# Kernel optimization log

Measured on AMD Instinct MI355X. Metric: run time of the kernel, lower is better.

Reference implementation:

```python
import jax, jax.numpy as jnp
import numpy as np

LN_EPS = 1e-5
L2_EPS = 1e-12
SCALE = 1.0 / np.sqrt(768.0)
TOPK = 8


def _ln(x, g, b):
    m = jnp.mean(x, axis=-1, keepdims=True)
    v = jnp.mean(jnp.square(x - m), axis=-1, keepdims=True)
    return (x - m) * jax.lax.rsqrt(v + LN_EPS) * g + b


def _l2norm(x):
    n = jnp.sqrt(jnp.sum(jnp.square(x), axis=-1, keepdims=True))
    return x / jnp.maximum(n, L2_EPS)


def _topk_normalize(scores, k):
    # scores: [B, K]; keep top-k, zero rest, renormalize to sum 1
    vals, idx = jax.lax.top_k(scores, k)
    B = scores.shape[0]
    weights = jnp.zeros_like(scores).at[jnp.arange(B)[:, None], idx].set(vals)
    denom = jnp.maximum(jnp.sum(weights, axis=1, keepdims=True), 1e-8)
    return weights / denom


def setup_inputs() -> dict:
    key = jax.random.key(0)
    ks = jax.random.split(key, 8)
    B, N, D, K, H, C = 32, 4096, 768, 64, 3072, 1000
    inp = {
        "patch_tokens": jax.random.normal(ks[0], (B, N, D), jnp.float32),
        "global_features": jax.random.normal(ks[1], (B, D), jnp.float32),
        "base_logits": jax.random.normal(ks[2], (B, C), jnp.float32),
        "bq": jax.random.normal(ks[3], (K, D), jnp.float32) * 0.02,
        "qn_g": jnp.ones((D,)), "qn_b": jnp.zeros((D,)),
        "tn_g": jnp.ones((D,)), "tn_b": jnp.zeros((D,)),
        "bn_g": jnp.ones((D,)), "bn_b": jnp.zeros((D,)),
        "gn_g": jnp.ones((D,)), "gn_b": jnp.zeros((D,)),
        "rln_g": jnp.ones((D,)), "rln_b": jnp.zeros((D,)),
        "rw1": jax.random.normal(ks[4], (D, H), jnp.float32) / np.sqrt(D),
        "rb1": jnp.zeros((H,)),
        "rw2": jax.random.normal(ks[5], (H, 1), jnp.float32) / np.sqrt(H),
        "rb2": jnp.zeros((1,)),
        "hw1": jax.random.normal(ks[6], (2 * D, H), jnp.float32) / np.sqrt(2 * D),
        "hb1": jnp.zeros((H,)),
        "hw2": jax.random.normal(ks[7], (H, C), jnp.float32) / np.sqrt(H),
        "hb2": jnp.zeros((C,)),
    }
    return inp


def reference(patch_tokens, global_features, base_logits, bq,
              qn_g, qn_b, tn_g, tn_b, bn_g, bn_b, gn_g, gn_b,
              rln_g, rln_b, rw1, rb1, rw2, rb2, hw1, hb1, hw2, hb2):
    # normalized cross-attention: K basis queries vs N tokens
    tokens_key = _l2norm(_ln(patch_tokens, tn_g, tn_b))           # [B,N,D]
    queries = _l2norm(_ln(bq, qn_g, qn_b))                        # [K,D]
    attn_logits = jnp.einsum('kd,bnd->bkn', queries, tokens_key) * SCALE
    attn_weights = jax.nn.softmax(attn_logits, axis=-1)           # [B,K,N]
    basis_states = jnp.einsum('bkn,bnd->bkd', attn_weights, patch_tokens)
    # routing head: LN -> Linear -> GELU -> Linear -> softplus
    r = _ln(basis_states, rln_g, rln_b)
    r = jax.nn.gelu(r @ rw1 + rb1, approximate=False)
    routing_scores = jax.nn.softplus((r @ rw2 + rb2)[..., 0])     # [B,K]
    routing_weights = _topk_normalize(routing_scores, TOPK)
    basis_summary = jnp.einsum('bk,bkd->bd', routing_weights, basis_states)
    basis_summary = _ln(basis_summary, bn_g, bn_b)
    global_summary = _ln(global_features, gn_g, gn_b)
    fused = jnp.concatenate([global_summary, basis_summary], axis=-1)
    h = jax.nn.gelu(fused @ hw1 + hb1, approximate=False)
    residual_logits = h @ hw2 + hb2
    final_logits = base_logits + residual_logits
    # diversity loss over basis queries
    bqn = _l2norm(bq)
    gram = bqn @ bqn.T
    diversity_loss = jnp.mean(jnp.square(gram - jnp.eye(gram.shape[0], dtype=gram.dtype)))
    sparse_loss = jnp.mean(routing_scores)
    return (final_logits, residual_logits, routing_weights, sparse_loss, diversity_loss)
```

## Files before the change

### kernel.cpp

```cpp
#include <hip/hip_runtime.h>
#include <math.h>

#define SCALE 0.036084391824351613f

typedef unsigned short us;
typedef __attribute__((ext_vector_type(8))) short short8;
typedef __attribute__((ext_vector_type(4))) short short4s;
typedef __attribute__((ext_vector_type(4))) float f32x4;
#define MFMA16(a, b, c) __builtin_amdgcn_mfma_f32_16x16x32_bf16(a, b, c, 0, 0, 0)

__device__ __forceinline__ us f2bf(float f) {
  unsigned u = __float_as_uint(f);
  unsigned r = (u + 0x7fffu + ((u >> 16) & 1u)) >> 16;
  return (us)r;
}
__device__ __forceinline__ float bf2f(us u) { return __uint_as_float(((unsigned)u) << 16); }

__device__ __forceinline__ void split8(f32x4 a, f32x4 b, short8& hi, short8& lo) {
  float x[8] = {a[0], a[1], a[2], a[3], b[0], b[1], b[2], b[3]};
#pragma unroll
  for (int i = 0; i < 8; i++) {
    us h = f2bf(x[i]);
    hi[i] = (short)h;
    lo[i] = (short)f2bf(x[i] - bf2f(h));
  }
}

__device__ __forceinline__ float blockReduceSum(float v, float* sh) {
#pragma unroll
  for (int o = 32; o > 0; o >>= 1) v += __shfl_xor(v, o, 64);
  int lane = threadIdx.x & 63, wid = threadIdx.x >> 6;
  __syncthreads();
  if (lane == 0) sh[wid] = v;
  __syncthreads();
  float r = sh[0];
  int nw = blockDim.x >> 6;
  for (int i = 1; i < nw; i++) r += sh[i];
  return r;
}

__device__ __forceinline__ float blockReduceMax(float v, float* sh) {
#pragma unroll
  for (int o = 32; o > 0; o >>= 1) v = fmaxf(v, __shfl_xor(v, o, 64));
  int lane = threadIdx.x & 63, wid = threadIdx.x >> 6;
  __syncthreads();
  if (lane == 0) sh[wid] = v;
  __syncthreads();
  float r = sh[0];
  int nw = blockDim.x >> 6;
  for (int i = 1; i < nw; i++) r = fmaxf(r, sh[i]);
  return r;
}

__device__ __forceinline__ float gelu_exact(float x) {
  return 0.5f * x * (1.0f + erff(x * 0.7071067811865476f));
}

__global__ void __launch_bounds__(256) k_prep_queries(
    const float* __restrict__ bq, const float* __restrict__ qn_g, const float* __restrict__ qn_b,
    const float* __restrict__ tn_g, const float* __restrict__ tn_b,
    us* __restrict__ qgh, us* __restrict__ qgl,
    float* __restrict__ s1, float* __restrict__ qb,
    float* __restrict__ bqn, float* __restrict__ gcons) {
  __shared__ float sh[8];
  int k = blockIdx.x, t = threadIdx.x;
  const float* xr = bq + (size_t)k * 768;
  float x0 = xr[t], x1 = xr[t + 256], x2 = xr[t + 512];
  float sx = blockReduceSum(x0 + x1 + x2, sh);
  float sxx = blockReduceSum(x0 * x0 + x1 * x1 + x2 * x2, sh);
  float mean = sx * (1.0f / 768.0f);
  float var = fmaxf(sxx * (1.0f / 768.0f) - mean * mean, 0.0f);
  float rs = rsqrtf(var + 1e-5f);
  float y0 = (x0 - mean) * rs * qn_g[t] + qn_b[t];
  float y1 = (x1 - mean) * rs * qn_g[t + 256] + qn_b[t + 256];
  float y2 = (x2 - mean) * rs * qn_g[t + 512] + qn_b[t + 512];
  float ss = blockReduceSum(y0 * y0 + y1 * y1 + y2 * y2, sh);
  float inv = 1.0f / fmaxf(sqrtf(ss), 1e-12f);
  float q0 = y0 * inv, q1 = y1 * inv, q2 = y2 * inv;
  float tg0 = tn_g[t], tg1 = tn_g[t + 256], tg2 = tn_g[t + 512];
  float tb0 = tn_b[t], tb1 = tn_b[t + 256], tb2 = tn_b[t + 512];
  float g0 = q0 * tg0, g1 = q1 * tg1, g2 = q2 * tg2;
  us h0 = f2bf(g0), h1 = f2bf(g1), h2 = f2bf(g2);
  qgh[(size_t)k * 768 + t] = h0;
  qgh[(size_t)k * 768 + t + 256] = h1;
  qgh[(size_t)k * 768 + t + 512] = h2;
  qgl[(size_t)k * 768 + t] = f2bf(g0 - bf2f(h0));
  qgl[(size_t)k * 768 + t + 256] = f2bf(g1 - bf2f(h1));
  qgl[(size_t)k * 768 + t + 512] = f2bf(g2 - bf2f(h2));
  float s1p = blockReduceSum(g0 + g1 + g2, sh);
  float qbp = blockReduceSum(q0 * tb0 + q1 * tb1 + q2 * tb2, sh);
  if (t == 0) { s1[k] = s1p; qb[k] = qbp; }
  float inv2 = 1.0f / fmaxf(sqrtf(sxx), 1e-12f);
  bqn[(size_t)k * 768 + t] = x0 * inv2;
  bqn[(size_t)k * 768 + t + 256] = x1 * inv2;
  bqn[(size_t)k * 768 + t + 512] = x2 * inv2;
  float sggp = blockReduceSum(tg0 * tg0 + tg1 * tg1 + tg2 * tg2, sh);
  float sgbp = blockReduceSum(tg0 * tb0 + tg1 * tb1 + tg2 * tb2, sh);
  float sbbp = blockReduceSum(tb0 * tb0 + tb1 * tb1 + tb2 * tb2, sh);
  if (k == 0 && t == 0) { gcons[0] = sggp; gcons[1] = sgbp; gcons[2] = sbbp; }
}

__global__ void __launch_bounds__(256) k_gram(const float* __restrict__ bqn,
                                              float* __restrict__ gpart) {
  __shared__ float bk[768];
  __shared__ float arr[64];
  int k = blockIdx.x, t = threadIdx.x;
  bk[t] = bqn[(size_t)k * 768 + t];
  bk[t + 256] = bqn[(size_t)k * 768 + t + 256];
  bk[t + 512] = bqn[(size_t)k * 768 + t + 512];
  __syncthreads();
  int j = t >> 2, sub = t & 3;
  const float* bj = bqn + (size_t)j * 768 + sub * 192;
  float v = 0.0f;
  for (int d = 0; d < 192; d++) v += bk[sub * 192 + d] * bj[d];
  v += __shfl_xor(v, 1, 64);
  v += __shfl_xor(v, 2, 64);
  if (sub == 0) { float e = v - (j == k ? 1.0f : 0.0f); arr[j] = e * e; }
  __syncthreads();
  if (t < 64) {
    float s = arr[t];
#pragma unroll
    for (int o = 32; o > 0; o >>= 1) s += __shfl_xor(s, o, 64);
    if (t == 0) gpart[k] = s;
  }
}

__global__ void __launch_bounds__(256) k_w1t(const float* __restrict__ rw1,
                                             us* __restrict__ w1th, us* __restrict__ w1tl) {
  __shared__ float tl[32][33];
  int d0 = blockIdx.x * 32, h0 = blockIdx.y * 32;
  int t = threadIdx.x, tx = t & 31, ty = t >> 5;
#pragma unroll
  for (int j = 0; j < 4; j++)
    tl[ty + j * 8][tx] = rw1[(size_t)(d0 + ty + j * 8) * 3072 + h0 + tx];
  __syncthreads();
#pragma unroll
  for (int j = 0; j < 4; j++) {
    float v = tl[tx][ty + j * 8];
    us h = f2bf(v);
    w1th[(size_t)(h0 + ty + j * 8) * 768 + d0 + tx] = h;
    w1tl[(size_t)(h0 + ty + j * 8) * 768 + d0 + tx] = f2bf(v - bf2f(h));
  }
}

__global__ void __launch_bounds__(256) k_attn_mfma(
    const float* __restrict__ x, const us* __restrict__ qgh, const us* __restrict__ qgl,
    const float* __restrict__ s1v, const float* __restrict__ qbv,
    const float* __restrict__ tng, const float* __restrict__ tnb,
    const float* __restrict__ gcons, float* __restrict__ L) {
  __shared__ __align__(16) us qsh[64 * 32], qsl[64 * 32];
  __shared__ __align__(16) us xsh[128 * 32], xsl[128 * 32];
  __shared__ float sA[128], sB[128], sC[128];
  const int b = blockIdx.y, n0 = blockIdx.x * 128;
  const int t = threadIdx.x, w = t >> 6, l = t & 63;
  const int sr = t >> 2, sq = t & 3;
  const us* qsrcH = qgh + (size_t)sr * 768 + sq * 8;
  const us* qsrcL = qgl + (size_t)sr * 768 + sq * 8;
  const float* xsrc = x + ((size_t)b * 4096 + n0 + sr) * 768 + sq * 8;
  f32x4 acc[4][2];
#pragma unroll
  for (int i = 0; i < 4; i++)
#pragma unroll
    for (int j = 0; j < 2; j++) acc[i][j] = (f32x4){0.f, 0.f, 0.f, 0.f};
  float s0x = 0, s0xx = 0, s0a = 0, s0b = 0, s0c = 0;
  float t1x = 0, t1xx = 0, t1a = 0, t1b = 0, t1c = 0;
  short8 qh = *(const short8*)qsrcH, ql = *(const short8*)qsrcL;
  f32x4 x0a = *(const f32x4*)xsrc, x0b = *(const f32x4*)(xsrc + 4);
  f32x4 x1a = *(const f32x4*)(xsrc + (size_t)64 * 768);
  f32x4 x1b = *(const f32x4*)(xsrc + (size_t)64 * 768 + 4);
  for (int dk = 0; dk < 768; dk += 32) {
    f32x4 ga = *(const f32x4*)(tng + dk + sq * 8);
    f32x4 gA = *(const f32x4*)(tng + dk + sq * 8 + 4);
    f32x4 ba = *(const f32x4*)(tnb + dk + sq * 8);
    f32x4 bA = *(const f32x4*)(tnb + dk + sq * 8 + 4);
#pragma unroll
    for (int i = 0; i < 4; i++) {
      float g1 = ga[i], g2 = gA[i], b1 = ba[i], b2 = bA[i];
      float xv = x0a[i]; float gx = g1 * xv;
      s0x += xv; s0xx = fmaf(xv, xv, s0xx);
      s0a = fmaf(gx, gx, s0a); s0b = fmaf(g1, gx, s0b); s0c = fmaf(b1, gx, s0c);
      xv = x0b[i]; gx = g2 * xv;
      s0x += xv; s0xx = fmaf(xv, xv, s0xx);
      s0a = fmaf(gx, gx, s0a); s0b = fmaf(g2, gx, s0b); s0c = fmaf(b2, gx, s0c);
      xv = x1a[i]; gx = g1 * xv;
      t1x += xv; t1xx = fmaf(xv, xv, t1xx);
      t1a = fmaf(gx, gx, t1a); t1b = fmaf(g1, gx, t1b); t1c = fmaf(b1, gx, t1c);
      xv = x1b[i]; gx = g2 * xv;
      t1x += xv; t1xx = fmaf(xv, xv, t1xx);
      t1a = fmaf(gx, gx, t1a); t1b = fmaf(g2, gx, t1b); t1c = fmaf(b2, gx, t1c);
    }
    short8 hi, lo;
    __syncthreads();
    *(short8*)&qsh[sr * 32 + sq * 8] = qh; *(short8*)&qsl[sr * 32 + sq * 8] = ql;
    split8(x0a, x0b, hi, lo);
    *(short8*)&xsh[sr * 32 + sq * 8] = hi; *(short8*)&xsl[sr * 32 + sq * 8] = lo;
    split8(x1a, x1b, hi, lo);
    *(short8*)&xsh[(sr + 64) * 32 + sq * 8] = hi; *(short8*)&xsl[(sr + 64) * 32 + sq * 8] = lo;
    __syncthreads();
    if (dk + 32 < 768) {
      int d2 = dk + 32;
      qh = *(const short8*)(qsrcH + d2); ql = *(const short8*)(qsrcL + d2);
      x0a = *(const f32x4*)(xsrc + d2); x0b = *(const f32x4*)(xsrc + d2 + 4);
      x1a = *(const f32x4*)(xsrc + (size_t)64 * 768 + d2);
      x1b = *(const f32x4*)(xsrc + (size_t)64 * 768 + d2 + 4);
    }
    short8 ah[4], al[4];
#pragma unroll
    for (int kt = 0; kt < 4; kt++) {
      int off = (kt * 16 + (l & 15)) * 32 + (l >> 4) * 8;
      ah[kt] = *(const short8*)&qsh[off];
      al[kt] = *(const short8*)&qsl[off];
    }
#pragma unroll
    for (int nt = 0; nt < 2; nt++) {
      int off = (w * 32 + nt * 16 + (l & 15)) * 32 + (l >> 4) * 8;
      short8 bh = *(const short8*)&xsh[off];
      short8 bl = *(const short8*)&xsl[off];
#pragma unroll
      for (int kt = 0; kt < 4; kt++) {
        acc[kt][nt] = MFMA16(ah[kt], bh, acc[kt][nt]);
        acc[kt][nt] = MFMA16(ah[kt], bl, acc[kt][nt]);
        acc[kt][nt] = MFMA16(al[kt], bh, acc[kt][nt]);
        acc[kt][nt] = MFMA16(al[kt], bl, acc[kt][nt]);
      }
    }
  }
  float sgg = gcons[0], sgb = gcons[1], sbb = gcons[2];
#define R4(v) v += __shfl_xor(v, 1, 64); v += __shfl_xor(v, 2, 64)
  R4(s0x); R4(s0xx); R4(s0a); R4(s0b); R4(s0c);
  R4(t1x); R4(t1xx); R4(t1a); R4(t1b); R4(t1c);
#undef R4
  if (sq == 0) {
    {
      float m = s0x * (1.0f / 768.0f);
      float var = fmaxf(s0xx * (1.0f / 768.0f) - m * m, 0.0f);
      float rs = rsqrtf(var + 1e-5f);
      float ss = fmaxf(rs * rs * (s0a - 2.0f * m * s0b + m * m * sgg) +
                       2.0f * rs * (s0c - m * sgb) + sbb, 0.0f);
      float inv = 1.0f / fmaxf(sqrtf(ss), 1e-12f);
      float A = SCALE * inv * rs;
      sA[sr] = A; sB[sr] = A * m; sC[sr] = SCALE * inv;
    }
    {
      float m = t1x * (1.0f / 768.0f);
      float var = fmaxf(t1xx * (1.0f / 768.0f) - m * m, 0.0f);
      float rs = rsqrtf(var + 1e-5f);
      float ss = fmaxf(rs * rs * (t1a - 2.0f * m * t1b + m * m * sgg) +
                       2.0f * rs * (t1c - m * sgb) + sbb, 0.0f);
      float inv = 1.0f / fmaxf(sqrtf(ss), 1e-12f);
      float A = SCALE * inv * rs;
      sA[sr + 64] = A; sB[sr + 64] = A * m; sC[sr + 64] = SCALE * inv;
    }
  }
  __syncthreads();
#pragma unroll
  for (int nt = 0; nt < 2; nt++) {
    int nn = w * 32 + nt * 16 + (l & 15);
    int n = n0 + nn;
    float Av = sA[nn], Bv = sB[nn], Cv = sC[nn];
#pragma unroll
    for (int kt = 0; kt < 4; kt++) {
#pragma unroll
      for (int r = 0; r < 4; r++) {
        int k = kt * 16 + (l >> 4) * 4 + r;
        L[((size_t)b * 64 + k) * 4096 + n] = Av * acc[kt][nt][r] - Bv * s1v[k] + Cv * qbv[k];
      }
    }
  }
}

__global__ void __launch_bounds__(256) k_rowstat(const float* __restrict__ L,
                                                 float* __restrict__ rowm,
                                                 float* __restrict__ rowinv) {
  __shared__ float sh[8];
  size_t row = blockIdx.x;
  const f32x4* p = (const f32x4*)(L + row * 4096);
  int t = threadIdx.x;
  f32x4 v[4];
  float mx = -INFINITY;
#pragma unroll
  for (int i = 0; i < 4; i++) {
    v[i] = p[t + i * 256];
#pragma unroll
    for (int j = 0; j < 4; j++) mx = fmaxf(mx, v[i][j]);
  }
  mx = blockReduceMax(mx, sh);
  float s = 0.0f;
#pragma unroll
  for (int i = 0; i < 4; i++)
#pragma unroll
    for (int j = 0; j < 4; j++) s += expf(v[i][j] - mx);
  s = blockReduceSum(s, sh);
  if (t == 0) { rowm[row] = mx; rowinv[row] = 1.0f / s; }
}

__global__ void __launch_bounds__(256) k_zero(float* __restrict__ p) {
  ((f32x4*)p)[blockIdx.x * 256 + threadIdx.x] = (f32x4){0.f, 0.f, 0.f, 0.f};
}

__global__ void __launch_bounds__(256) k_pv_mfma(
    const float* __restrict__ x, const float* __restrict__ W,
    const float* __restrict__ rowm, const float* __restrict__ rowinv,
    float* __restrict__ S) {
  __shared__ __align__(16) us wth[64 * 32], wtl[64 * 32];
  __shared__ __align__(16) us xth[8 * 32 * 16], xtl[8 * 32 * 16];
  const int b = blockIdx.y, d0 = blockIdx.x * 128, nb = blockIdx.z * 512;
  const int t = threadIdx.x, w = t >> 6, l = t & 63;
  const int krow = t >> 2;
  const float* wsrc = W + ((size_t)b * 64 + krow) * 4096 + nb + (t & 3) * 8;
  const float mr = rowm[b * 64 + krow];
  const float ir = rowinv[b * 64 + krow];
  const int gg = t >> 6, nn = (t >> 1) & 31, hh = t & 1;
  const float* xsrc0 = x + ((size_t)b * 4096 + nb + nn) * 768 + d0 + gg * 16 + hh * 8;
  const float* xsrc1 = xsrc0 + 64;
  f32x4 acc[4][2];
#pragma unroll
  for (int i = 0; i < 4; i++)
#pragma unroll
    for (int j = 0; j < 2; j++) acc[i][j] = (f32x4){0.f, 0.f, 0.f, 0.f};
  f32x4 w0a = *(const f32x4*)wsrc, w0b = *(const f32x4*)(wsrc + 4);
  f32x4 xa0 = *(const f32x4*)xsrc0, xb0 = *(const f32x4*)(xsrc0 + 4);
  f32x4 xa1 = *(const f32x4*)xsrc1, xb1 = *(const f32x4*)(xsrc1 + 4);
  for (int ns = 0; ns < 512; ns += 32) {
    short8 hi, lo;
    f32x4 e0, e1;
#pragma unroll
    for (int i = 0; i < 4; i++) {
      e0[i] = expf(w0a[i] - mr) * ir;
      e1[i] = expf(w0b[i] - mr) * ir;
    }
    __syncthreads();
    split8(e0, e1, hi, lo);
    *(short8*)&wth[krow * 32 + (t & 3) * 8] = hi;
    *(short8*)&wtl[krow * 32 + (t & 3) * 8] = lo;
    split8(xa0, xb0, hi, lo);
    *(short8*)&xth[(size_t)t * 8] = hi; *(short8*)&xtl[(size_t)t * 8] = lo;
    split8(xa1, xb1, hi, lo);
    *(short8*)&xth[((size_t)t + 256) * 8] = hi; *(short8*)&xtl[((size_t)t + 256) * 8] = lo;
    __syncthreads();
    if (ns + 32 < 512) {
      w0a = *(const f32x4*)(wsrc + ns + 32); w0b = *(const f32x4*)(wsrc + ns + 36);
      const float* p0 = xsrc0 + (size_t)(ns + 32) * 768;
      xa0 = *(const f32x4*)p0; xb0 = *(const f32x4*)(p0 + 4);
      xa1 = *(const f32x4*)(p0 + 64); xb1 = *(const f32x4*)(p0 + 68);
    }
    short8 ah[4], al[4];
#pragma unroll
    for (int kt = 0; kt < 4; kt++) {
      int off = (kt * 16 + (l & 15)) * 32 + (l >> 4) * 8;
      ah[kt] = *(const short8*)&wth[off];
      al[kt] = *(const short8*)&wtl[off];
    }
#pragma unroll
    for (int dt = 0; dt < 2; dt++) {
      const us* gph = &xth[(2 * w + dt) * 512];
      const us* gpl = &xtl[(2 * w + dt) * 512];
      int rb = (l >> 4) * 8, cc = l & 15;
      short8 bh, bl;
#pragma unroll
      for (int i = 0; i < 8; i++) {
        bh[i] = (short)gph[(rb + i) * 16 + cc];
        bl[i] = (short)gpl[(rb + i) * 16 + cc];
      }
#pragma unroll
      for (int kt = 0; kt < 4; kt++) {
        acc[kt][dt] = MFMA16(ah[kt], bh, acc[kt][dt]);
        acc[kt][dt] = MFMA16(ah[kt], bl, acc[kt][dt]);
        acc[kt][dt] = MFMA16(al[kt], bh, acc[kt][dt]);
        acc[kt][dt] = MFMA16(al[kt], bl, acc[kt][dt]);
      }
    }
  }
#pragma unroll
  for (int dt = 0; dt < 2; dt++) {
    int d = d0 + w * 32 + dt * 16 + (l & 15);
#pragma unroll
    for (int kt = 0; kt < 4; kt++) {
#pragma unroll
      for (int r = 0; r < 4; r++) {
        int k = kt * 16 + (l >> 4) * 4 + r;
        atomicAdd(&S[((size_t)b * 64 + k) * 768 + d], acc[kt][dt][r]);
      }
    }
  }
}

__global__ void __launch_bounds__(256) k_ln768(
    const float* __restrict__ in, const float* __restrict__ g, const float* __restrict__ b,
    us* __restrict__ outh, us* __restrict__ outl) {
  int wid = threadIdx.x >> 6, lane = threadIdx.x & 63;
  size_t row = (size_t)blockIdx.x * 4 + wid;
  const f32x4* xr = (const f32x4*)(in + row * 768);
  f32x4 v[3];
  float sx = 0, sxx = 0;
#pragma unroll
  for (int j = 0; j < 3; j++) {
    v[j] = xr[lane + j * 64];
#pragma unroll
    for (int i = 0; i < 4; i++) { sx += v[j][i]; sxx = fmaf(v[j][i], v[j][i], sxx); }
  }
#pragma unroll
  for (int o = 32; o > 0; o >>= 1) { sx += __shfl_xor(sx, o, 64); sxx += __shfl_xor(sxx, o, 64); }
  float mean = sx * (1.0f / 768.0f);
  float var = fmaxf(sxx * (1.0f / 768.0f) - mean * mean, 0.0f);
  float rs = rsqrtf(var + 1e-5f);
  const f32x4* gp = (const f32x4*)g;
  const f32x4* bp = (const f32x4*)b;
#pragma unroll
  for (int j = 0; j < 3; j++) {
    f32x4 gv = gp[lane + j * 64], bv = bp[lane + j * 64];
    short4s h4, l4;
#pragma unroll
    for (int i = 0; i < 4; i++) {
      float y = (v[j][i] - mean) * rs * gv[i] + bv[i];
      us h = f2bf(y);
      h4[i] = (short)h;
      l4[i] = (short)f2bf(y - bf2f(h));
    }
    int e = (lane + j * 64) * 4;
    *(short4s*)&outh[row * 768 + e] = h4;
    *(short4s*)&outl[row * 768 + e] = l4;
  }
}

__global__ void __launch_bounds__(256) k_rh_mfma(
    const us* __restrict__ rhh, const us* __restrict__ rhl,
    const us* __restrict__ w1th, const us* __restrict__ w1tl,
    const float* __restrict__ rb1, const float* __restrict__ rw2,
    float* __restrict__ scores_raw) {
  __shared__ __align__(16) us ash[64 * 32], asl[64 * 32];
  __shared__ __align__(16) us bsh[128 * 32], bsl[128 * 32];
  __shared__ float spart[4][64];
  const int h0 = blockIdx.x * 128, m0 = blockIdx.y * 64;
  const int t = threadIdx.x, w = t >> 6, l = t & 63;
  const int sr = t >> 2, sq = t & 3;
  const us* aH = rhh + (size_t)(m0 + sr) * 768 + sq * 8;
  const us* aL = rhl + (size_t)(m0 + sr) * 768 + sq * 8;
  const us* bH = w1th + (size_t)(h0 + sr) * 768 + sq * 8;
  const us* bL = w1tl + (size_t)(h0 + sr) * 768 + sq * 8;
  f32x4 acc[4][2];
#pragma unroll
  for (int i = 0; i < 4; i++)
#pragma unroll
    for (int j = 0; j < 2; j++) acc[i][j] = (f32x4){0.f, 0.f, 0.f, 0.f};
  short8 a0h = *(const short8*)aH, a0l = *(const short8*)aL;
  short8 b0h = *(const short8*)bH, b0l = *(const short8*)bL;
  short8 b1h = *(const short8*)(bH + (size_t)64 * 768);
  short8 b1l = *(const short8*)(bL + (size_t)64 * 768);
  for (int dk = 0; dk < 768; dk += 32) {
    __syncthreads();
    *(short8*)&ash[sr * 32 + sq * 8] = a0h; *(short8*)&asl[sr * 32 + sq * 8] = a0l;
    *(short8*)&bsh[sr * 32 + sq * 8] = b0h; *(short8*)&bsl[sr * 32 + sq * 8] = b0l;
    *(short8*)&bsh[(sr + 64) * 32 + sq * 8] = b1h; *(short8*)&bsl[(sr + 64) * 32 + sq * 8] = b1l;
    __syncthreads();
    if (dk + 32 < 768) {
      int d2 = dk + 32;
      a0h = *(const short8*)(aH + d2); a0l = *(const short8*)(aL + d2);
      b0h = *(const short8*)(bH + d2); b0l = *(const short8*)(bL + d2);
      b1h = *(const short8*)(bH + (size_t)64 * 768 + d2);
      b1l = *(const short8*)(bL + (size_t)64 * 768 + d2);
    }
    short8 ah[4], al[4];
#pragma unroll
    for (int kt = 0; kt < 4; kt++) {
      int off = (kt * 16 + (l & 15)) * 32 + (l >> 4) * 8;
      ah[kt] = *(const short8*)&ash[off];
      al[kt] = *(const short8*)&asl[off];
    }
#pragma unroll
    for (int nt = 0; nt < 2; nt++) {
      int off = (w * 32 + nt * 16 + (l & 15)) * 32 + (l >> 4) * 8;
      short8 bh = *(const short8*)&bsh[off];
      short8 bl = *(const short8*)&bsl[off];
#pragma unroll
      for (int kt = 0; kt < 4; kt++) {
        acc[kt][nt] = MFMA16(ah[kt], bh, acc[kt][nt]);
        acc[kt][nt] = MFMA16(ah[kt], bl, acc[kt][nt]);
        acc[kt][nt] = MFMA16(al[kt], bh, acc[kt][nt]);
        acc[kt][nt] = MFMA16(al[kt], bl, acc[kt][nt]);
      }
    }
  }
  float psum[4][4];
#pragma unroll
  for (int kt = 0; kt < 4; kt++)
#pragma unroll
    for (int r = 0; r < 4; r++) psum[kt][r] = 0.f;
#pragma unroll
  for (int nt = 0; nt < 2; nt++) {
    int h = h0 + w * 32 + nt * 16 + (l & 15);
    float bias = rb1[h];
    float rw2v = rw2[h];
#pragma unroll
    for (int kt = 0; kt < 4; kt++) {
#pragma unroll
      for (int r = 0; r < 4; r++) {
        float g = gelu_exact(acc[kt][nt][r] + bias);
        psum[kt][r] = fmaf(g, rw2v, psum[kt][r]);
      }
    }
  }
#pragma unroll
  for (int kt = 0; kt < 4; kt++)
#pragma unroll
    for (int r = 0; r < 4; r++) {
      float v = psum[kt][r];
      v += __shfl_xor(v, 1, 64);
      v += __shfl_xor(v, 2, 64);
      v += __shfl_xor(v, 4, 64);
      v += __shfl_xor(v, 8, 64);
      psum[kt][r] = v;
    }
  if ((l & 15) == 0) {
#pragma unroll
    for (int kt = 0; kt < 4; kt++)
#pragma unroll
      for (int r = 0; r < 4; r++)
        spart[w][kt * 16 + (l >> 4) * 4 + r] = psum[kt][r];
  }
  __syncthreads();
  if (t < 64)
    atomicAdd(&scores_raw[m0 + t], spart[0][t] + spart[1][t] + spart[2][t] + spart[3][t]);
}

__global__ void __launch_bounds__(256) k_fused(
    const float* __restrict__ bs, const float* __restrict__ scores_raw,
    const float* __restrict__ rb2, const float* __restrict__ gf,
    const float* __restrict__ bn_g, const float* __restrict__ bn_b,
    const float* __restrict__ gn_g, const float* __restrict__ gn_b,
    float* __restrict__ fused, float* __restrict__ rw_out) {
  __shared__ float sh[8];
  __shared__ float wsh[64];
  int b = blockIdx.x, t = threadIdx.x;
  if (t < 64) {
    float z = scores_raw[b * 64 + t] + rb2[0];
    float s = fmaxf(z, 0.0f) + log1pf(expf(-fabsf(z)));
    bool sel = false;
    for (int it = 0; it < 8; it++) {
      float v = sel ? -INFINITY : s;
      int idx = t;
#pragma unroll
      for (int o = 32; o > 0; o >>= 1) {
        float v2 = __shfl_xor(v, o, 64);
        int i2 = __shfl_xor(idx, o, 64);
        if (v2 > v || (v2 == v && i2 < idx)) { v = v2; idx = i2; }
      }
      if (t == idx) sel = true;
    }
    float wv = sel ? s : 0.0f;
    float tot = wv;
#pragma unroll
    for (int o = 32; o > 0; o >>= 1) tot += __shfl_xor(tot, o, 64);
    float wt = wv / fmaxf(tot, 1e-8f);
    wsh[t] = wt;
    rw_out[b * 64 + t] = wt;
  }
  __syncthreads();
  float v0 = 0, v1 = 0, v2 = 0;
  const float* bsb = bs + (size_t)b * 64 * 768;
  for (int k = 0; k < 64; k++) {
    float w = wsh[k];
    if (w != 0.0f) {
      v0 = fmaf(w, bsb[(size_t)k * 768 + t], v0);
      v1 = fmaf(w, bsb[(size_t)k * 768 + t + 256], v1);
      v2 = fmaf(w, bsb[(size_t)k * 768 + t + 512], v2);
    }
  }
  float sx = blockReduceSum(v0 + v1 + v2, sh);
  float sxx = blockReduceSum(v0 * v0 + v1 * v1 + v2 * v2, sh);
  float mean = sx * (1.0f / 768.0f);
  float var = fmaxf(sxx * (1.0f / 768.0f) - mean * mean, 0.0f);
  float rs = rsqrtf(var + 1e-5f);
  float* fb = fused + (size_t)b * 1536;
  fb[768 + t] = (v0 - mean) * rs * bn_g[t] + bn_b[t];
  fb[768 + t + 256] = (v1 - mean) * rs * bn_g[t + 256] + bn_b[t + 256];
  fb[768 + t + 512] = (v2 - mean) * rs * bn_g[t + 512] + bn_b[t + 512];
  const float* gr = gf + (size_t)b * 768;
  float g0 = gr[t], g1 = gr[t + 256], g2 = gr[t + 512];
  float gsx = blockReduceSum(g0 + g1 + g2, sh);
  float gsxx = blockReduceSum(g0 * g0 + g1 * g1 + g2 * g2, sh);
  float gm = gsx * (1.0f / 768.0f);
  float gv = fmaxf(gsxx * (1.0f / 768.0f) - gm * gm, 0.0f);
  float grs = rsqrtf(gv + 1e-5f);
  fb[t] = (g0 - gm) * grs * gn_g[t] + gn_b[t];
  fb[t + 256] = (g1 - gm) * grs * gn_g[t + 256] + gn_b[t + 256];
  fb[t + 512] = (g2 - gm) * grs * gn_g[t + 512] + gn_b[t + 512];
}

__global__ void __launch_bounds__(256) k_head1(
    const float* __restrict__ fused, const float* __restrict__ hw1, const float* __restrict__ hb1,
    float* __restrict__ h) {
  __shared__ float fl[2][1536];
  __shared__ float part[2][4][64];
  int bp = blockIdx.y * 2, h0 = blockIdx.x * 64, t = threadIdx.x;
  for (int i = t; i < 1536; i += 256) {
    fl[0][i] = fused[(size_t)bp * 1536 + i];
    fl[1][i] = fused[(size_t)(bp + 1) * 1536 + i];
  }
  __syncthreads();
  int c = t & 63, sl = t >> 6;
  int hh = h0 + c;
  int kbase = sl * 384;
  const float* wp = hw1 + (size_t)kbase * 3072 + hh;
  float a0 = 0.f, a1 = 0.f;
#pragma unroll 8
  for (int k = 0; k < 384; k++) {
    float w = wp[(size_t)k * 3072];
    a0 = fmaf(fl[0][kbase + k], w, a0);
    a1 = fmaf(fl[1][kbase + k], w, a1);
  }
  part[0][sl][c] = a0; part[1][sl][c] = a1;
  __syncthreads();
  if (sl == 0) {
    float bias = hb1[hh];
    float s0 = part[0][0][c] + part[0][1][c] + part[0][2][c] + part[0][3][c];
    float s1_ = part[1][0][c] + part[1][1][c] + part[1][2][c] + part[1][3][c];
    h[(size_t)bp * 3072 + hh] = gelu_exact(s0 + bias);
    h[(size_t)(bp + 1) * 3072 + hh] = gelu_exact(s1_ + bias);
  }
}

__global__ void __launch_bounds__(256) k_head2(
    const float* __restrict__ h, const float* __restrict__ hw2, const float* __restrict__ hb2,
    const float* __restrict__ base, float* __restrict__ out) {
  __shared__ float hl[2][3072];
  __shared__ float part[2][4][64];
  int bp = blockIdx.y * 2, c0 = blockIdx.x * 64, t = threadIdx.x;
  for (int i = t; i < 3072; i += 256) {
    hl[0][i] = h[(size_t)bp * 3072 + i];
    hl[1][i] = h[(size_t)(bp + 1) * 3072 + i];
  }
  __syncthreads();
  int c = t & 63, sl = t >> 6;
  int cc = c0 + c;
  int csafe = cc < 1000 ? cc : 999;
  int kbase = sl * 768;
  const float* wp = hw2 + (size_t)kbase * 1000 + csafe;
  float a0 = 0.f, a1 = 0.f;
#pragma unroll 8
  for (int k = 0; k < 768; k++) {
    float w = wp[(size_t)k * 1000];
    a0 = fmaf(hl[0][kbase + k], w, a0);
    a1 = fmaf(hl[1][kbase + k], w, a1);
  }
  part[0][sl][c] = a0; part[1][sl][c] = a1;
  __syncthreads();
  if (sl == 0 && cc < 1000) {
    float bias = hb2[cc];
    float s0 = part[0][0][c] + part[0][1][c] + part[0][2][c] + part[0][3][c] + bias;
    float s1_ = part[1][0][c] + part[1][1][c] + part[1][2][c] + part[1][3][c] + bias;
    out[32000 + bp * 1000 + cc] = s0;
    out[bp * 1000 + cc] = base[bp * 1000 + cc] + s0;
    out[32000 + (bp + 1) * 1000 + cc] = s1_;
    out[(bp + 1) * 1000 + cc] = base[(bp + 1) * 1000 + cc] + s1_;
  }
}

__global__ void __launch_bounds__(256) k_losses(
    const float* __restrict__ scores_raw, const float* __restrict__ rb2,
    const float* __restrict__ gpart, float* __restrict__ out) {
  __shared__ float sh[8];
  int t = threadIdx.x;
  float s = 0.0f;
#pragma unroll
  for (int i = 0; i < 8; i++) {
    float z = scores_raw[t + i * 256] + rb2[0];
    s += fmaxf(z, 0.0f) + log1pf(expf(-fabsf(z)));
  }
  s = blockReduceSum(s, sh);
  float gsum = (t < 64) ? gpart[t] : 0.0f;
  gsum = blockReduceSum(gsum, sh);
  if (t == 0) {
    out[66048] = s * (1.0f / 2048.0f);
    out[66049] = gsum * (1.0f / 4096.0f);
  }
}

extern "C" void kernel_launch(void* const* d_in, const int* in_sizes, int n_in,
                              void* d_out, int out_size, void* d_ws, size_t ws_size,
                              hipStream_t stream) {
  const float* patch = (const float*)d_in[0];
  const float* gfeat = (const float*)d_in[1];
  const float* base  = (const float*)d_in[2];
  const float* bq    = (const float*)d_in[3];
  const float* qn_g  = (const float*)d_in[4];
  const float* qn_b  = (const float*)d_in[5];
  const float* tn_g  = (const float*)d_in[6];
  const float* tn_b  = (const float*)d_in[7];
  const float* bn_g  = (const float*)d_in[8];
  const float* bn_b  = (const float*)d_in[9];
  const float* gn_g  = (const float*)d_in[10];
  const float* gn_b  = (const float*)d_in[11];
  const float* rln_g = (const float*)d_in[12];
  const float* rln_b = (const float*)d_in[13];
  const float* rw1   = (const float*)d_in[14];
  const float* rb1   = (const float*)d_in[15];
  const float* rw2   = (const float*)d_in[16];
  const float* rb2   = (const float*)d_in[17];
  const float* hw1   = (const float*)d_in[18];
  const float* hb1   = (const float*)d_in[19];
  const float* hw2   = (const float*)d_in[20];
  const float* hb2   = (const float*)d_in[21];
  float* ws = (float*)d_ws;
  float* out = (float*)d_out;

  float* s1      = ws + 0;
  float* qb      = ws + 64;
  float* gcons   = ws + 128;
  float* gpart   = ws + 160;
  float* rowm    = ws + 224;
  float* rowinv  = ws + 2272;
  float* fusedb  = ws + 4320;
  float* hbuf    = ws + 53472;
  float* bqn     = ws + 151776;
  us*    qgh     = (us*)(ws + 200928);
  us*    qgl     = (us*)(ws + 225504);
  us*    w1th    = (us*)(ws + 250080);
  us*    w1tl    = (us*)(ws + 1429728);
  us*    rhh     = (us*)(ws + 2609376);
  us*    rhl     = (us*)(ws + 3395808);
  float* bs      = ws + 4182240;
  float* scores  = ws + 5755104;
  float* L       = ws + 5757152;

  k_prep_queries<<<dim3(64), 256, 0, stream>>>(bq, qn_g, qn_b, tn_g, tn_b,
                                               qgh, qgl, s1, qb, bqn, gcons);
  k_gram<<<dim3(64), 256, 0, stream>>>(bqn, gpart);
  k_w1t<<<dim3(24, 96), 256, 0, stream>>>(rw1, w1th, w1tl);
  k_attn_mfma<<<dim3(32, 32), 256, 0, stream>>>(patch, qgh, qgl, s1, qb, tn_g, tn_b, gcons, L);
  k_rowstat<<<dim3(2048), 256, 0, stream>>>(L, rowm, rowinv);
  k_zero<<<dim3(1538), 256, 0, stream>>>(bs);
  k_pv_mfma<<<dim3(6, 32, 8), 256, 0, stream>>>(patch, L, rowm, rowinv, bs);
  k_ln768<<<dim3(512), 256, 0, stream>>>(bs, rln_g, rln_b, rhh, rhl);
  k_rh_mfma<<<dim3(24, 32), 256, 0, stream>>>(rhh, rhl, w1th, w1tl, rb1, rw2, scores);
  k_fused<<<dim3(32), 256, 0, stream>>>(bs, scores, rb2, gfeat, bn_g, bn_b, gn_g, gn_b,
                                        fusedb, out + 64000);
  k_head1<<<dim3(48, 16), 256, 0, stream>>>(fusedb, hw1, hb1, hbuf);
  k_head2<<<dim3(16, 16), 256, 0, stream>>>(hbuf, hw2, hb2, base, out);
  k_losses<<<dim3(1), 256, 0, stream>>>(scores, rb2, gpart, out);
}
```

Measured before the change: 422.5 us.

## Fuse softmax row sums into attention kernel, widen PV, RH and head1 tiles

The separate row-statistics kernel is removed. The attention kernel now accumulates exp(logit) row sums with shuffles and atomics, relying on the logits being bounded by the L2-normalised cosine scale, so no max subtraction is needed. The PV kernel covers 256 feature columns per block instead of 128, halving redundant exp and split work on the weights. The routing-head MFMA kernel uses 512 threads and 128-row tiles, and head1 processes four batch rows per block to reuse weight loads. Together these trade extra register and LDS pressure, plus reliance on bounded logits, for fewer passes over the logits and fewer launches.

```diff
diff --git a/kernel.cpp b/kernel.cpp
--- a/kernel.cpp
+++ b/kernel.cpp
@@ -36,19 +36,6 @@
   float r = sh[0];
   int nw = blockDim.x >> 6;
   for (int i = 1; i < nw; i++) r += sh[i];
-  return r;
-}
-
-__device__ __forceinline__ float blockReduceMax(float v, float* sh) {
-#pragma unroll
-  for (int o = 32; o > 0; o >>= 1) v = fmaxf(v, __shfl_xor(v, o, 64));
-  int lane = threadIdx.x & 63, wid = threadIdx.x >> 6;
-  __syncthreads();
-  if (lane == 0) sh[wid] = v;
-  __syncthreads();
-  float r = sh[0];
-  int nw = blockDim.x >> 6;
-  for (int i = 1; i < nw; i++) r = fmaxf(r, sh[i]);
   return r;
 }
 
@@ -147,10 +134,11 @@
     const float* __restrict__ x, const us* __restrict__ qgh, const us* __restrict__ qgl,
     const float* __restrict__ s1v, const float* __restrict__ qbv,
     const float* __restrict__ tng, const float* __restrict__ tnb,
-    const float* __restrict__ gcons, float* __restrict__ L) {
+    const float* __restrict__ gcons, float* __restrict__ L, float* __restrict__ rowsum) {
   __shared__ __align__(16) us qsh[64 * 32], qsl[64 * 32];
   __shared__ __align__(16) us xsh[128 * 32], xsl[128 * 32];
   __shared__ float sA[128], sB[128], sC[128];
+  __shared__ float sRow[4][64];
   const int b = blockIdx.y, n0 = blockIdx.x * 128;
   const int t = threadIdx.x, w = t >> 6, l = t & 63;
   const int sr = t >> 2, sq = t & 3;
@@ -253,6 +241,11 @@
     }
   }
   __syncthreads();
+  float esum[4][4];
+#pragma unroll
+  for (int kt = 0; kt < 4; kt++)
+#pragma unroll
+    for (int r = 0; r < 4; r++) esum[kt][r] = 0.f;
 #pragma unroll
   for (int nt = 0; nt < 2; nt++) {
     int nn = w * 32 + nt * 16 + (l & 15);
@@ -263,35 +256,26 @@
 #pragma unroll
       for (int r = 0; r < 4; r++) {
         int k = kt * 16 + (l >> 4) * 4 + r;
-        L[((size_t)b * 64 + k) * 4096 + n] = Av * acc[kt][nt][r] - Bv * s1v[k] + Cv * qbv[k];
-      }
-    }
-  }
-}
-
-__global__ void __launch_bounds__(256) k_rowstat(const float* __restrict__ L,
-                                                 float* __restrict__ rowm,
-                                                 float* __restrict__ rowinv) {
-  __shared__ float sh[8];
-  size_t row = blockIdx.x;
-  const f32x4* p = (const f32x4*)(L + row * 4096);
-  int t = threadIdx.x;
-  f32x4 v[4];
-  float mx = -INFINITY;
-#pragma unroll
-  for (int i = 0; i < 4; i++) {
-    v[i] = p[t + i * 256];
-#pragma unroll
-    for (int j = 0; j < 4; j++) mx = fmaxf(mx, v[i][j]);
-  }
-  mx = blockReduceMax(mx, sh);
-  float s = 0.0f;
-#pragma unroll
-  for (int i = 0; i < 4; i++)
-#pragma unroll
-    for (int j = 0; j < 4; j++) s += expf(v[i][j] - mx);
-  s = blockReduceSum(s, sh);
-  if (t == 0) { rowm[row] = mx; rowinv[row] = 1.0f / s; }
+        float v = Av * acc[kt][nt][r] - Bv * s1v[k] + Cv * qbv[k];
+        L[((size_t)b * 64 + k) * 4096 + n] = v;
+        esum[kt][r] += expf(v);
+      }
+    }
+  }
+#pragma unroll
+  for (int kt = 0; kt < 4; kt++)
+#pragma unroll
+    for (int r = 0; r < 4; r++) {
+      float e = esum[kt][r];
+      e += __shfl_xor(e, 1, 64);
+      e += __shfl_xor(e, 2, 64);
+      e += __shfl_xor(e, 4, 64);
+      e += __shfl_xor(e, 8, 64);
+      if ((l & 15) == 0) sRow[w][kt * 16 + (l >> 4) * 4 + r] = e;
+    }
+  __syncthreads();
+  if (t < 64)
+    atomicAdd(&rowsum[b * 64 + t], sRow[0][t] + sRow[1][t] + sRow[2][t] + sRow[3][t]);
 }
 
 __global__ void __launch_bounds__(256) k_zero(float* __restrict__ p) {
@@ -300,49 +284,56 @@
 
 __global__ void __launch_bounds__(256) k_pv_mfma(
     const float* __restrict__ x, const float* __restrict__ W,
-    const float* __restrict__ rowm, const float* __restrict__ rowinv,
-    float* __restrict__ S) {
+    const float* __restrict__ rowsum, float* __restrict__ S) {
   __shared__ __align__(16) us wth[64 * 32], wtl[64 * 32];
-  __shared__ __align__(16) us xth[8 * 32 * 16], xtl[8 * 32 * 16];
-  const int b = blockIdx.y, d0 = blockIdx.x * 128, nb = blockIdx.z * 512;
+  __shared__ __align__(16) us xth[16 * 32 * 16], xtl[16 * 32 * 16];
+  const int b = blockIdx.y, d0 = blockIdx.x * 256, nb = blockIdx.z * 512;
   const int t = threadIdx.x, w = t >> 6, l = t & 63;
   const int krow = t >> 2;
   const float* wsrc = W + ((size_t)b * 64 + krow) * 4096 + nb + (t & 3) * 8;
-  const float mr = rowm[b * 64 + krow];
-  const float ir = rowinv[b * 64 + krow];
+  const float ir = 1.0f / rowsum[b * 64 + krow];
   const int gg = t >> 6, nn = (t >> 1) & 31, hh = t & 1;
-  const float* xsrc0 = x + ((size_t)b * 4096 + nb + nn) * 768 + d0 + gg * 16 + hh * 8;
-  const float* xsrc1 = xsrc0 + 64;
-  f32x4 acc[4][2];
+  const float* xbase = x + ((size_t)b * 4096 + nb + nn) * 768 + d0 + gg * 16 + hh * 8;
+  f32x4 acc[4][4];
 #pragma unroll
   for (int i = 0; i < 4; i++)
 #pragma unroll
-    for (int j = 0; j < 2; j++) acc[i][j] = (f32x4){0.f, 0.f, 0.f, 0.f};
+    for (int j = 0; j < 4; j++) acc[i][j] = (f32x4){0.f, 0.f, 0.f, 0.f};
   f32x4 w0a = *(const f32x4*)wsrc, w0b = *(const f32x4*)(wsrc + 4);
-  f32x4 xa0 = *(const f32x4*)xsrc0, xb0 = *(const f32x4*)(xsrc0 + 4);
-  f32x4 xa1 = *(const f32x4*)xsrc1, xb1 = *(const f32x4*)(xsrc1 + 4);
+  f32x4 xa[4], xb[4];
+#pragma unroll
+  for (int j = 0; j < 4; j++) {
+    xa[j] = *(const f32x4*)(xbase + 64 * j);
+    xb[j] = *(const f32x4*)(xbase + 64 * j + 4);
+  }
   for (int ns = 0; ns < 512; ns += 32) {
     short8 hi, lo;
     f32x4 e0, e1;
 #pragma unroll
     for (int i = 0; i < 4; i++) {
-      e0[i] = expf(w0a[i] - mr) * ir;
-      e1[i] = expf(w0b[i] - mr) * ir;
+      e0[i] = expf(w0a[i]) * ir;
+      e1[i] = expf(w0b[i]) * ir;
     }
     __syncthreads();
     split8(e0, e1, hi, lo);
     *(short8*)&wth[krow * 32 + (t & 3) * 8] = hi;
     *(short8*)&wtl[krow * 32 + (t & 3) * 8] = lo;
-    split8(xa0, xb0, hi, lo);
-    *(short8*)&xth[(size_t)t * 8] = hi; *(short8*)&xtl[(size_t)t * 8] = lo;
-    split8(xa1, xb1, hi, lo);
-    *(short8*)&xth[((size_t)t + 256) * 8] = hi; *(short8*)&xtl[((size_t)t + 256) * 8] = lo;
+#pragma unroll
+    for (int j = 0; j < 4; j++) {
+      split8(xa[j], xb[j], hi, lo);
+      size_t xoff = ((size_t)(gg + 4 * j) * 32 + nn) * 16 + hh * 8;
+      *(short8*)&xth[xoff] = hi;
+      *(short8*)&xtl[xoff] = lo;
+    }
     __syncthreads();
     if (ns + 32 < 512) {
       w0a = *(const f32x4*)(wsrc + ns + 32); w0b = *(const f32x4*)(wsrc + ns + 36);
-      const float* p0 = xsrc0 + (size_t)(ns + 32) * 768;
-      xa0 = *(const f32x4*)p0; xb0 = *(const f32x4*)(p0 + 4);
-      xa1 = *(const f32x4*)(p0 + 64); xb1 = *(const f32x4*)(p0 + 68);
+      const float* p0 = xbase + (size_t)(ns + 32) * 768;
+#pragma unroll
+      for (int j = 0; j < 4; j++) {
+        xa[j] = *(const f32x4*)(p0 + 64 * j);
+        xb[j] = *(const f32x4*)(p0 + 64 * j + 4);
+      }
     }
     short8 ah[4], al[4];
 #pragma unroll
@@ -352,9 +343,9 @@
       al[kt] = *(const short8*)&wtl[off];
     }
 #pragma unroll
-    for (int dt = 0; dt < 2; dt++) {
-      const us* gph = &xth[(2 * w + dt) * 512];
-      const us* gpl = &xtl[(2 * w + dt) * 512];
+    for (int dt = 0; dt < 4; dt++) {
+      const us* gph = &xth[(4 * w + dt) * 512];
+      const us* gpl = &xtl[(4 * w + dt) * 512];
       int rb = (l >> 4) * 8, cc = l & 15;
       short8 bh, bl;
 #pragma unroll
@@ -372,8 +363,8 @@
     }
   }
 #pragma unroll
-  for (int dt = 0; dt < 2; dt++) {
-    int d = d0 + w * 32 + dt * 16 + (l & 15);
+  for (int dt = 0; dt < 4; dt++) {
+    int d = d0 + w * 64 + dt * 16 + (l & 15);
 #pragma unroll
     for (int kt = 0; kt < 4; kt++) {
 #pragma unroll
@@ -423,16 +414,17 @@
   }
 }
 
-__global__ void __launch_bounds__(256) k_rh_mfma(
+__global__ void __launch_bounds__(512) k_rh_mfma(
     const us* __restrict__ rhh, const us* __restrict__ rhl,
     const us* __restrict__ w1th, const us* __restrict__ w1tl,
     const float* __restrict__ rb1, const float* __restrict__ rw2,
     float* __restrict__ scores_raw) {
-  __shared__ __align__(16) us ash[64 * 32], asl[64 * 32];
+  __shared__ __align__(16) us ash[128 * 32], asl[128 * 32];
   __shared__ __align__(16) us bsh[128 * 32], bsl[128 * 32];
-  __shared__ float spart[4][64];
-  const int h0 = blockIdx.x * 128, m0 = blockIdx.y * 64;
+  __shared__ float spart[4][128];
+  const int h0 = blockIdx.x * 128, m0 = blockIdx.y * 128;
   const int t = threadIdx.x, w = t >> 6, l = t & 63;
+  const int wm = w >> 2, wh = w & 3;
   const int sr = t >> 2, sq = t & 3;
   const us* aH = rhh + (size_t)(m0 + sr) * 768 + sq * 8;
   const us* aL = rhl + (size_t)(m0 + sr) * 768 + sq * 8;
@@ -445,31 +437,26 @@
     for (int j = 0; j < 2; j++) acc[i][j] = (f32x4){0.f, 0.f, 0.f, 0.f};
   short8 a0h = *(const short8*)aH, a0l = *(const short8*)aL;
   short8 b0h = *(const short8*)bH, b0l = *(const short8*)bL;
-  short8 b1h = *(const short8*)(bH + (size_t)64 * 768);
-  short8 b1l = *(const short8*)(bL + (size_t)64 * 768);
   for (int dk = 0; dk < 768; dk += 32) {
     __syncthreads();
     *(short8*)&ash[sr * 32 + sq * 8] = a0h; *(short8*)&asl[sr * 32 + sq * 8] = a0l;
     *(short8*)&bsh[sr * 32 + sq * 8] = b0h; *(short8*)&bsl[sr * 32 + sq * 8] = b0l;
-    *(short8*)&bsh[(sr + 64) * 32 + sq * 8] = b1h; *(short8*)&bsl[(sr + 64) * 32 + sq * 8] = b1l;
     __syncthreads();
     if (dk + 32 < 768) {
       int d2 = dk + 32;
       a0h = *(const short8*)(aH + d2); a0l = *(const short8*)(aL + d2);
       b0h = *(const short8*)(bH + d2); b0l = *(const short8*)(bL + d2);
-      b1h = *(const short8*)(bH + (size_t)64 * 768 + d2);
-      b1l = *(const short8*)(bL + (size_t)64 * 768 + d2);
     }
     short8 ah[4], al[4];
 #pragma unroll
     for (int kt = 0; kt < 4; kt++) {
-      int off = (kt * 16 + (l & 15)) * 32 + (l >> 4) * 8;
+      int off = ((wm * 64 + kt * 16 + (l & 15))) * 32 + (l >> 4) * 8;
       ah[kt] = *(const short8*)&ash[off];
       al[kt] = *(const short8*)&asl[off];
     }
 #pragma unroll
     for (int nt = 0; nt < 2; nt++) {
-      int off = (w * 32 + nt * 16 + (l & 15)) * 32 + (l >> 4) * 8;
+      int off = ((wh * 32 + nt * 16 + (l & 15))) * 32 + (l >> 4) * 8;
       short8 bh = *(const short8*)&bsh[off];
       short8 bl = *(const short8*)&bsl[off];
 #pragma unroll
@@ -488,7 +475,7 @@
     for (int r = 0; r < 4; r++) psum[kt][r] = 0.f;
 #pragma unroll
   for (int nt = 0; nt < 2; nt++) {
-    int h = h0 + w * 32 + nt * 16 + (l & 15);
+    int h = h0 + wh * 32 + nt * 16 + (l & 15);
     float bias = rb1[h];
     float rw2v = rw2[h];
 #pragma unroll
@@ -509,17 +496,10 @@
       v += __shfl_xor(v, 2, 64);
       v += __shfl_xor(v, 4, 64);
       v += __shfl_xor(v, 8, 64);
-      psum[kt][r] = v;
-    }
-  if ((l & 15) == 0) {
-#pragma unroll
-    for (int kt = 0; kt < 4; kt++)
-#pragma unroll
-      for (int r = 0; r < 4; r++)
-        spart[w][kt * 16 + (l >> 4) * 4 + r] = psum[kt][r];
-  }
-  __syncthreads();
-  if (t < 64)
+      if ((l & 15) == 0) spart[wh][wm * 64 + kt * 16 + (l >> 4) * 4 + r] = v;
+    }
+  __syncthreads();
+  if (t < 128)
     atomicAdd(&scores_raw[m0 + t], spart[0][t] + spart[1][t] + spart[2][t] + spart[3][t]);
 }
 
@@ -590,33 +570,36 @@
 __global__ void __launch_bounds__(256) k_head1(
     const float* __restrict__ fused, const float* __restrict__ hw1, const float* __restrict__ hb1,
     float* __restrict__ h) {
-  __shared__ float fl[2][1536];
-  __shared__ float part[2][4][64];
-  int bp = blockIdx.y * 2, h0 = blockIdx.x * 64, t = threadIdx.x;
+  __shared__ float fl[4][1536];
+  __shared__ float part[4][4][64];
+  int bp = blockIdx.y * 4, h0 = blockIdx.x * 64, t = threadIdx.x;
   for (int i = t; i < 1536; i += 256) {
-    fl[0][i] = fused[(size_t)bp * 1536 + i];
-    fl[1][i] = fused[(size_t)(bp + 1) * 1536 + i];
+#pragma unroll
+    for (int j = 0; j < 4; j++) fl[j][i] = fused[(size_t)(bp + j) * 1536 + i];
   }
   __syncthreads();
   int c = t & 63, sl = t >> 6;
   int hh = h0 + c;
   int kbase = sl * 384;
   const float* wp = hw1 + (size_t)kbase * 3072 + hh;
-  float a0 = 0.f, a1 = 0.f;
+  float a0 = 0.f, a1 = 0.f, a2 = 0.f, a3 = 0.f;
 #pragma unroll 8
   for (int k = 0; k < 384; k++) {
     float w = wp[(size_t)k * 3072];
     a0 = fmaf(fl[0][kbase + k], w, a0);
     a1 = fmaf(fl[1][kbase + k], w, a1);
-  }
-  part[0][sl][c] = a0; part[1][sl][c] = a1;
+    a2 = fmaf(fl[2][kbase + k], w, a2);
+    a3 = fmaf(fl[3][kbase + k], w, a3);
+  }
+  part[0][sl][c] = a0; part[1][sl][c] = a1; part[2][sl][c] = a2; part[3][sl][c] = a3;
   __syncthreads();
   if (sl == 0) {
     float bias = hb1[hh];
-    float s0 = part[0][0][c] + part[0][1][c] + part[0][2][c] + part[0][3][c];
-    float s1_ = part[1][0][c] + part[1][1][c] + part[1][2][c] + part[1][3][c];
-    h[(size_t)bp * 3072 + hh] = gelu_exact(s0 + bias);
-    h[(size_t)(bp + 1) * 3072 + hh] = gelu_exact(s1_ + bias);
+#pragma unroll
+    for (int j = 0; j < 4; j++) {
+      float s = part[j][0][c] + part[j][1][c] + part[j][2][c] + part[j][3][c];
+      h[(size_t)(bp + j) * 3072 + hh] = gelu_exact(s + bias);
+    }
   }
 }
 
@@ -708,34 +691,33 @@
   float* qb      = ws + 64;
   float* gcons   = ws + 128;
   float* gpart   = ws + 160;
-  float* rowm    = ws + 224;
-  float* rowinv  = ws + 2272;
-  float* fusedb  = ws + 4320;
-  float* hbuf    = ws + 53472;
-  float* bqn     = ws + 151776;
-  us*    qgh     = (us*)(ws + 200928);
-  us*    qgl     = (us*)(ws + 225504);
-  us*    w1th    = (us*)(ws + 250080);
-  us*    w1tl    = (us*)(ws + 1429728);
-  us*    rhh     = (us*)(ws + 2609376);
-  us*    rhl     = (us*)(ws + 3395808);
-  float* bs      = ws + 4182240;
-  float* scores  = ws + 5755104;
-  float* L       = ws + 5757152;
+  float* fusedb  = ws + 224;
+  float* hbuf    = ws + 49376;
+  float* bqn     = ws + 147680;
+  us*    qgh     = (us*)(ws + 196832);
+  us*    qgl     = (us*)(ws + 221408);
+  us*    w1th    = (us*)(ws + 245984);
+  us*    w1tl    = (us*)(ws + 1425632);
+  us*    rhh     = (us*)(ws + 2605280);
+  us*    rhl     = (us*)(ws + 3391712);
+  float* bs      = ws + 4178144;
+  float* scores  = ws + 5751008;
+  float* rowsum  = ws + 5753056;
+  float* L       = ws + 5755104;
 
   k_prep_queries<<<dim3(64), 256, 0, stream>>>(bq, qn_g, qn_b, tn_g, tn_b,
                                                qgh, qgl, s1, qb, bqn, gcons);
   k_gram<<<dim3(64), 256, 0, stream>>>(bqn, gpart);
   k_w1t<<<dim3(24, 96), 256, 0, stream>>>(rw1, w1th, w1tl);
-  k_attn_mfma<<<dim3(32, 32), 256, 0, stream>>>(patch, qgh, qgl, s1, qb, tn_g, tn_b, gcons, L);
-  k_rowstat<<<dim3(2048), 256, 0, stream>>>(L, rowm, rowinv);
-  k_zero<<<dim3(1538), 256, 0, stream>>>(bs);
-  k_pv_mfma<<<dim3(6, 32, 8), 256, 0, stream>>>(patch, L, rowm, rowinv, bs);
+  k_zero<<<dim3(1540), 256, 0, stream>>>(bs);
+  k_attn_mfma<<<dim3(32, 32), 256, 0, stream>>>(patch, qgh, qgl, s1, qb, tn_g, tn_b,
+                                                gcons, L, rowsum);
+  k_pv_mfma<<<dim3(3, 32, 8), 256, 0, stream>>>(patch, L, rowsum, bs);
   k_ln768<<<dim3(512), 256, 0, stream>>>(bs, rln_g, rln_b, rhh, rhl);
-  k_rh_mfma<<<dim3(24, 32), 256, 0, stream>>>(rhh, rhl, w1th, w1tl, rb1, rw2, scores);
+  k_rh_mfma<<<dim3(24, 16), 512, 0, stream>>>(rhh, rhl, w1th, w1tl, rb1, rw2, scores);
   k_fused<<<dim3(32), 256, 0, stream>>>(bs, scores, rb2, gfeat, bn_g, bn_b, gn_g, gn_b,
                                         fusedb, out + 64000);
-  k_head1<<<dim3(48, 16), 256, 0, stream>>>(fusedb, hw1, hb1, hbuf);
+  k_head1<<<dim3(48, 8), 256, 0, stream>>>(fusedb, hw1, hb1, hbuf);
   k_head2<<<dim3(16, 16), 256, 0, stream>>>(hbuf, hw2, hb2, base, out);
   k_losses<<<dim3(1), 256, 0, stream>>>(scores, rb2, gpart, out);
 }
```

Measured after the change: 430.8 us. No clear change (+2.0%).
